# Optimization experiments

Hardware: AMD Instinct MI355X
Metric: run time of the kernel (lower is better)

## Reference

```python
import jax, jax.numpy as jnp
import numpy as np

N = 131072
F_IN = 256
FEATURES = 64
N_SOURCES = 32


def setup_inputs() -> dict:
    key = jax.random.key(0)
    k1, k2, k3 = jax.random.split(key, 3)
    x = jax.random.normal(k1, (N, F_IN), dtype=jnp.float32)
    source = jax.random.randint(k2, (N,), 0, N_SOURCES, dtype=jnp.int32)
    W = jax.random.normal(k3, (F_IN, N_SOURCES * FEATURES), dtype=jnp.float32) * (1.0 / np.sqrt(F_IN))
    b = jnp.zeros((N_SOURCES * FEATURES,), dtype=jnp.float32)
    return {"x": x, "source": source, "W": W, "b": b}


def reference(x, source, W, b):
    # Dense projection to all sources: (N, n_sources*features)
    y = jnp.dot(x, W) + b
    # Per-row gather of the slice belonging to this row's source id.
    # Equivalent to y[i, source[i]*FEATURES : (source[i]+1)*FEATURES].
    y = y.reshape(x.shape[0], N_SOURCES, FEATURES)
    out = jnp.take_along_axis(y, source[:, None, None].astype(jnp.int32), axis=1)
    return out[:, 0, :]  # (N, FEATURES)
```

## Files before the change

kernel.cpp:

```cpp
#include <hip/hip_runtime.h>

#define N_ROWS   131072
#define F_IN     256
#define FEAT     64
#define NSRC     32
#define WSTRIDE  (NSRC * FEAT)
#define CHUNK    4096
#define NCHUNK   (N_ROWS / CHUNK)
#define LCAP     320
#define KPAD     264
#define LCAP1    512

typedef __attribute__((ext_vector_type(8))) short  bf16x8;
typedef __attribute__((ext_vector_type(4))) float  f32x4;

__device__ __forceinline__ unsigned short f2bf(float f) {
    union { float f; unsigned u; } c; c.f = f;
    unsigned r = c.u + 0x7fffu + ((c.u >> 16) & 1u);
    return (unsigned short)(r >> 16);
}

__device__ __forceinline__ bf16x8 pack8(f32x4 f0, f32x4 f1) {
    bf16x8 a;
    a[0] = (short)f2bf(f0[0]); a[1] = (short)f2bf(f0[1]);
    a[2] = (short)f2bf(f0[2]); a[3] = (short)f2bf(f0[3]);
    a[4] = (short)f2bf(f1[0]); a[5] = (short)f2bf(f1[1]);
    a[6] = (short)f2bf(f1[2]); a[7] = (short)f2bf(f1[3]);
    return a;
}

__global__ __launch_bounds__(256)
void compact_kernel(const int* __restrict__ src, int* __restrict__ ws) {
    __shared__ int cnt[NSRC];
    __shared__ int lst[NSRC][LCAP];
    const int tid = threadIdx.x;
    if (tid < NSRC) cnt[tid] = 0;
    __syncthreads();

    const int chunk0 = blockIdx.x * CHUNK;
    #pragma unroll
    for (int r = 0; r < CHUNK / 256; ++r) {
        const int row = chunk0 + r * 256 + tid;
        const int s   = src[row];
        const int p   = atomicAdd(&cnt[s], 1);
        if (p < LCAP) lst[s][p] = row;
    }
    __syncthreads();

    if (tid < NSRC) ws[blockIdx.x * NSRC + tid] = min(cnt[tid], LCAP);
    int* gl = ws + NCHUNK * NSRC;
    for (int s = 0; s < NSRC; ++s) {
        const int c = min(cnt[s], LCAP);
        for (int i = tid; i < c; i += 256)
            gl[((size_t)blockIdx.x * NSRC + s) * LCAP + i] = lst[s][i];
    }
}

__global__ __launch_bounds__(256, 4)
void gemm_kernel(const float* __restrict__ x, const float* __restrict__ W,
                 const float* __restrict__ b, const int* __restrict__ ws,
                 float* __restrict__ out) {
    __shared__ __align__(16) unsigned short Wt[FEAT][KPAD];
    __shared__ int lst[LCAP];

    const int tid    = threadIdx.x;
    const int c      = blockIdx.x;
    const int s      = blockIdx.y;
    const int bucket = c * NSRC + s;
    const int count  = min(ws[bucket], LCAP);
    if (count == 0) return;

    for (int i = tid; i < count; i += 256)
        lst[i] = ws[NCHUNK * NSRC + (size_t)bucket * LCAP + i];

    {
        const int n  = tid & 63;
        const int kp = (tid >> 6) * 2;
        #pragma unroll
        for (int k0 = 0; k0 < F_IN; k0 += 8) {
            const int k = k0 + kp;
            const float w0 = W[(size_t)k       * WSTRIDE + s * FEAT + n];
            const float w1 = W[(size_t)(k + 1) * WSTRIDE + s * FEAT + n];
            *(unsigned*)&Wt[n][k] = (unsigned)f2bf(w0) | ((unsigned)f2bf(w1) << 16);
        }
    }
    __syncthreads();

    const int lane = tid & 63;
    const int w    = tid >> 6;
    const int col  = lane & 15;
    const int quad = lane >> 4;

    float bias[4];
    #pragma unroll
    for (int nt = 0; nt < 4; ++nt) bias[nt] = b[s * FEAT + nt * 16 + col];

    const int npass = (count + 63) >> 6;
    for (int p = 0; p < npass; ++p) {
        const int base = p * 64 + w * 16;
        const int ia   = lst[min(base + col, count - 1)];
        const float* ap = x + (size_t)ia * F_IN + quad * 8;

        f32x4 av[16];
        #pragma unroll
        for (int kk = 0; kk < 8; ++kk) {
            av[2 * kk]     = *(const f32x4*)(ap + kk * 32);
            av[2 * kk + 1] = *(const f32x4*)(ap + kk * 32 + 4);
        }

        f32x4 acc[4];
        #pragma unroll
        for (int nt = 0; nt < 4; ++nt) acc[nt] = (f32x4){0.f, 0.f, 0.f, 0.f};

        #pragma unroll
        for (int kk = 0; kk < 8; ++kk) {
            const bf16x8 a = pack8(av[2 * kk], av[2 * kk + 1]);
            #pragma unroll
            for (int nt = 0; nt < 4; ++nt) {
                const bf16x8 bb = *(const bf16x8*)&Wt[nt * 16 + col][kk * 32 + quad * 8];
                acc[nt] = __builtin_amdgcn_mfma_f32_16x16x32_bf16(a, bb, acc[nt], 0, 0, 0);
            }
        }

        #pragma unroll
        for (int reg = 0; reg < 4; ++reg) {
            const int gm = base + quad * 4 + reg;
            if (gm < count) {
                const int row = lst[gm];
                float* op = out + (size_t)row * FEAT;
                #pragma unroll
                for (int nt = 0; nt < 4; ++nt)
                    op[nt * 16 + col] = acc[nt][reg] + bias[nt];
            }
        }
    }
}

__global__ __launch_bounds__(256, 4)
void mono_kernel(const float* __restrict__ x, const int* __restrict__ src,
                 const float* __restrict__ W, const float* __restrict__ b,
                 float* __restrict__ out) {
    __shared__ __align__(16) unsigned short Wt[FEAT][KPAD];
    __shared__ int lst[LCAP1];
    __shared__ int cnt;

    const int tid    = threadIdx.x;
    const int s      = blockIdx.y;
    const int chunk0 = blockIdx.x * CHUNK;
    if (tid == 0) cnt = 0;
    __syncthreads();
    {
        const int n  = tid & 63;
        const int kp = (tid >> 6) * 2;
        #pragma unroll
        for (int k0 = 0; k0 < F_IN; k0 += 8) {
            const int k = k0 + kp;
            const float w0 = W[(size_t)k       * WSTRIDE + s * FEAT + n];
            const float w1 = W[(size_t)(k + 1) * WSTRIDE + s * FEAT + n];
            *(unsigned*)&Wt[n][k] = (unsigned)f2bf(w0) | ((unsigned)f2bf(w1) << 16);
        }
    }
    #pragma unroll
    for (int r = 0; r < CHUNK / 256; ++r) {
        const int row = chunk0 + r * 256 + tid;
        if (src[row] == s) {
            const int p = atomicAdd(&cnt, 1);
            if (p < LCAP1) lst[p] = row;
        }
    }
    __syncthreads();
    const int count = cnt;
    if (count == 0) return;
    const int lane = tid & 63, w = tid >> 6, col = lane & 15, quad = lane >> 4;
    float bias[4];
    #pragma unroll
    for (int nt = 0; nt < 4; ++nt) bias[nt] = b[s * FEAT + nt * 16 + col];
    const int npass = (count + 63) >> 6;
    for (int p = 0; p < npass; ++p) {
        const int base = p * 64 + w * 16;
        const int ia = lst[min(base + col, count - 1)];
        const float* ap = x + (size_t)ia * F_IN + quad * 8;
        f32x4 av[16];
        #pragma unroll
        for (int kk = 0; kk < 8; ++kk) {
            av[2 * kk]     = *(const f32x4*)(ap + kk * 32);
            av[2 * kk + 1] = *(const f32x4*)(ap + kk * 32 + 4);
        }
        f32x4 acc[4];
        #pragma unroll
        for (int nt = 0; nt < 4; ++nt) acc[nt] = (f32x4){0.f, 0.f, 0.f, 0.f};
        #pragma unroll
        for (int kk = 0; kk < 8; ++kk) {
            const bf16x8 a = pack8(av[2 * kk], av[2 * kk + 1]);
            #pragma unroll
            for (int nt = 0; nt < 4; ++nt) {
                const bf16x8 bb = *(const bf16x8*)&Wt[nt * 16 + col][kk * 32 + quad * 8];
                acc[nt] = __builtin_amdgcn_mfma_f32_16x16x32_bf16(a, bb, acc[nt], 0, 0, 0);
            }
        }
        #pragma unroll
        for (int reg = 0; reg < 4; ++reg) {
            const int gm = base + quad * 4 + reg;
            if (gm < count) {
                const int row = lst[gm];
                float* op = out + (size_t)row * FEAT;
                #pragma unroll
                for (int nt = 0; nt < 4; ++nt)
                    op[nt * 16 + col] = acc[nt][reg] + bias[nt];
            }
        }
    }
}

extern "C" void kernel_launch(void* const* d_in, const int* in_sizes, int n_in,
                              void* d_out, int out_size, void* d_ws, size_t ws_size,
                              hipStream_t stream) {
    const float* x   = (const float*)d_in[0];
    const int*   src = (const int*)d_in[1];
    const float* W   = (const float*)d_in[2];
    const float* b   = (const float*)d_in[3];
    float*       out = (float*)d_out;

    const size_t ws_needed = (size_t)(NCHUNK * NSRC) * (1 + LCAP) * sizeof(int);
    if (ws_size >= ws_needed) {
        int* ws = (int*)d_ws;
        compact_kernel<<<dim3(NCHUNK), dim3(256), 0, stream>>>(src, ws);
        gemm_kernel<<<dim3(NCHUNK, NSRC), dim3(256), 0, stream>>>(x, W, b, ws, out);
    } else {
        mono_kernel<<<dim3(NCHUNK, NSRC), dim3(256), 0, stream>>>(x, src, W, b, out);
    }
}
```

Measured before the change: 258.1 us.

## Double-buffer gathered x rows into LDS via async global_load_lds with register-held weights

Restructures the bucketed GEMM. Compaction now runs over many small blocks that reserve slots in global per-bucket counters with atomics, after a new zeroing kernel. Buckets grow to 8192-row chunks, giving fewer and larger GEMM blocks. The GEMM keeps the bf16 weight fragments in registers and streams gathered x rows into LDS with global_load_lds, double-buffered per wave and synchronised with waitcnt. Output is staged through LDS so rows are written with coalesced stores. The aim is to hide gather latency and improve store coalescing, at the cost of one wave set per CU (launch bounds 1), an extra kernel launch, and global atomics.

```diff
diff --git a/kernel.cpp b/kernel.cpp
--- a/kernel.cpp
+++ b/kernel.cpp
@@ -5,10 +5,16 @@
 #define FEAT     64
 #define NSRC     32
 #define WSTRIDE  (NSRC * FEAT)
-#define CHUNK    4096
-#define NCHUNK   (N_ROWS / CHUNK)
-#define LCAP     320
+#define NCH      16
+#define CHUNK    8192
+#define LCAP     640
+#define NBUCK    (NCH * NSRC)
 #define KPAD     264
+#define RSTRIDE  260
+#define BUFF     (16 * RSTRIDE)
+#define POOLF    (8 * BUFF)
+
+#define MCHUNK   4096
 #define LCAP1    512
 
 typedef __attribute__((ext_vector_type(8))) short  bf16x8;
@@ -29,38 +35,50 @@
     return a;
 }
 
+__device__ __forceinline__ void stage16(const float* __restrict__ x, int vr,
+                                        float* buf, int lane) {
+    #pragma unroll
+    for (int r = 0; r < 16; ++r) {
+        const int row = __builtin_amdgcn_readlane(vr, r);
+        const float* g = x + (size_t)row * F_IN + lane * 4;
+        __builtin_amdgcn_global_load_lds(
+            (const __attribute__((address_space(1))) void*)g,
+            (__attribute__((address_space(3))) void*)(buf + r * RSTRIDE),
+            16, 0, 0);
+    }
+}
+
+__global__ void zero_counts(int* __restrict__ ws) {
+    const int i = blockIdx.x * 256 + threadIdx.x;
+    if (i < NBUCK) ws[i] = 0;
+}
+
 __global__ __launch_bounds__(256)
 void compact_kernel(const int* __restrict__ src, int* __restrict__ ws) {
-    __shared__ int cnt[NSRC];
-    __shared__ int lst[NSRC][LCAP];
+    __shared__ int lcnt[NSRC];
+    __shared__ int gbase[NSRC];
     const int tid = threadIdx.x;
-    if (tid < NSRC) cnt[tid] = 0;
-    __syncthreads();
-
-    const int chunk0 = blockIdx.x * CHUNK;
-    #pragma unroll
-    for (int r = 0; r < CHUNK / 256; ++r) {
-        const int row = chunk0 + r * 256 + tid;
-        const int s   = src[row];
-        const int p   = atomicAdd(&cnt[s], 1);
-        if (p < LCAP) lst[s][p] = row;
-    }
-    __syncthreads();
-
-    if (tid < NSRC) ws[blockIdx.x * NSRC + tid] = min(cnt[tid], LCAP);
-    int* gl = ws + NCHUNK * NSRC;
-    for (int s = 0; s < NSRC; ++s) {
-        const int c = min(cnt[s], LCAP);
-        for (int i = tid; i < c; i += 256)
-            gl[((size_t)blockIdx.x * NSRC + s) * LCAP + i] = lst[s][i];
-    }
-}
-
-__global__ __launch_bounds__(256, 4)
+    if (tid < NSRC) lcnt[tid] = 0;
+    __syncthreads();
+
+    const int row = blockIdx.x * 256 + tid;
+    const int s   = src[row];
+    const int c   = (blockIdx.x * 256) >> 13;
+    const int p   = atomicAdd(&lcnt[s], 1);
+    __syncthreads();
+    if (tid < NSRC && lcnt[tid] > 0)
+        gbase[tid] = atomicAdd(&ws[c * NSRC + tid], lcnt[tid]);
+    __syncthreads();
+    const int pos = gbase[s] + p;
+    if (pos < LCAP)
+        ws[NBUCK + ((size_t)(c * NSRC + s)) * LCAP + pos] = row;
+}
+
+__global__ __launch_bounds__(256, 1)
 void gemm_kernel(const float* __restrict__ x, const float* __restrict__ W,
                  const float* __restrict__ b, const int* __restrict__ ws,
                  float* __restrict__ out) {
-    __shared__ __align__(16) unsigned short Wt[FEAT][KPAD];
+    __shared__ __align__(16) float pool[POOLF];
     __shared__ int lst[LCAP];
 
     const int tid    = threadIdx.x;
@@ -70,9 +88,10 @@
     const int count  = min(ws[bucket], LCAP);
     if (count == 0) return;
 
-    for (int i = tid; i < count; i += 256)
-        lst[i] = ws[NCHUNK * NSRC + (size_t)bucket * LCAP + i];
-
+    const int* gl = ws + NBUCK + (size_t)bucket * LCAP;
+    for (int i = tid; i < count; i += 256) lst[i] = gl[i];
+
+    unsigned short* Wt = (unsigned short*)pool;
     {
         const int n  = tid & 63;
         const int kp = (tid >> 6) * 2;
@@ -81,37 +100,134 @@
             const int k = k0 + kp;
             const float w0 = W[(size_t)k       * WSTRIDE + s * FEAT + n];
             const float w1 = W[(size_t)(k + 1) * WSTRIDE + s * FEAT + n];
+            *(unsigned*)&Wt[n * KPAD + k] = (unsigned)f2bf(w0) | ((unsigned)f2bf(w1) << 16);
+        }
+    }
+    __syncthreads();
+
+    const int lane = tid & 63, w = tid >> 6;
+    const int col  = lane & 15, quad = lane >> 4;
+
+    bf16x8 bfrag[4][8];
+    #pragma unroll
+    for (int nt = 0; nt < 4; ++nt)
+        #pragma unroll
+        for (int kk = 0; kk < 8; ++kk)
+            bfrag[nt][kk] = *(const bf16x8*)&Wt[(nt * 16 + col) * KPAD + kk * 32 + quad * 8];
+
+    float bias[4];
+    #pragma unroll
+    for (int nt = 0; nt < 4; ++nt) bias[nt] = b[s * FEAT + nt * 16 + col];
+
+    __syncthreads();
+
+    const int ntt = (count + 15) >> 4;
+    const int ntw = (w < ntt) ? (((ntt - 1 - w) >> 2) + 1) : 0;
+    if (ntw == 0) return;
+
+    float* buf0 = pool + w * (2 * BUFF);
+    float* buf1 = buf0 + BUFF;
+
+    __builtin_amdgcn_s_waitcnt(0x0F70);
+
+    int vr_cur = lst[min(w * 16 + col, count - 1)];
+    stage16(x, vr_cur, buf0, lane);
+
+    for (int i = 0; i < ntw; ++i) {
+        const int t    = w + 4 * i;
+        float*    bufc = (i & 1) ? buf1 : buf0;
+        const bool has_next = (i + 1 < ntw);
+        const bool has_prev = (i > 0);
+        int vr_next = 0;
+        if (has_next) {
+            vr_next = lst[min((t + 4) * 16 + col, count - 1)];
+            stage16(x, vr_next, (i & 1) ? buf0 : buf1, lane);
+        }
+        if (has_prev && has_next)      __builtin_amdgcn_s_waitcnt(0x8F70);
+        else if (has_prev || has_next) __builtin_amdgcn_s_waitcnt(0x4F70);
+        else                           __builtin_amdgcn_s_waitcnt(0x0F70);
+
+        f32x4 acc[4];
+        #pragma unroll
+        for (int nt = 0; nt < 4; ++nt) acc[nt] = (f32x4){0.f, 0.f, 0.f, 0.f};
+
+        #pragma unroll
+        for (int kk = 0; kk < 8; ++kk) {
+            const float* ap = bufc + col * RSTRIDE + kk * 32 + quad * 8;
+            const f32x4 a0 = *(const f32x4*)ap;
+            const f32x4 a1 = *(const f32x4*)(ap + 4);
+            const bf16x8 a = pack8(a0, a1);
+            #pragma unroll
+            for (int nt = 0; nt < 4; ++nt)
+                acc[nt] = __builtin_amdgcn_mfma_f32_16x16x32_bf16(a, bfrag[nt][kk], acc[nt], 0, 0, 0);
+        }
+
+        #pragma unroll
+        for (int nt = 0; nt < 4; ++nt)
+            #pragma unroll
+            for (int reg = 0; reg < 4; ++reg)
+                bufc[(quad * 4 + reg) * 65 + nt * 16 + col] = acc[nt][reg] + bias[nt];
+        #pragma unroll
+        for (int r = 0; r < 16; ++r) {
+            const int gi = t * 16 + r;
+            if (gi < count) {
+                const int row = __builtin_amdgcn_readlane(vr_cur, r);
+                out[(size_t)row * FEAT + lane] = bufc[r * 65 + lane];
+            }
+        }
+        vr_cur = vr_next;
+    }
+}
+
+__global__ __launch_bounds__(256, 4)
+void mono_kernel(const float* __restrict__ x, const int* __restrict__ src,
+                 const float* __restrict__ W, const float* __restrict__ b,
+                 float* __restrict__ out) {
+    __shared__ __align__(16) unsigned short Wt[FEAT][KPAD];
+    __shared__ int lst[LCAP1];
+    __shared__ int cnt;
+    const int tid = threadIdx.x, s = blockIdx.y, chunk0 = blockIdx.x * MCHUNK;
+    if (tid == 0) cnt = 0;
+    __syncthreads();
+    {
+        const int n = tid & 63, kp = (tid >> 6) * 2;
+        #pragma unroll
+        for (int k0 = 0; k0 < F_IN; k0 += 8) {
+            const int k = k0 + kp;
+            const float w0 = W[(size_t)k * WSTRIDE + s * FEAT + n];
+            const float w1 = W[(size_t)(k + 1) * WSTRIDE + s * FEAT + n];
             *(unsigned*)&Wt[n][k] = (unsigned)f2bf(w0) | ((unsigned)f2bf(w1) << 16);
         }
     }
-    __syncthreads();
-
-    const int lane = tid & 63;
-    const int w    = tid >> 6;
-    const int col  = lane & 15;
-    const int quad = lane >> 4;
-
+    #pragma unroll
+    for (int r = 0; r < MCHUNK / 256; ++r) {
+        const int row = chunk0 + r * 256 + tid;
+        if (src[row] == s) {
+            const int p = atomicAdd(&cnt, 1);
+            if (p < LCAP1) lst[p] = row;
+        }
+    }
+    __syncthreads();
+    const int count = cnt;
+    if (count == 0) return;
+    const int lane = tid & 63, w = tid >> 6, col = lane & 15, quad = lane >> 4;
     float bias[4];
     #pragma unroll
     for (int nt = 0; nt < 4; ++nt) bias[nt] = b[s * FEAT + nt * 16 + col];
-
     const int npass = (count + 63) >> 6;
     for (int p = 0; p < npass; ++p) {
         const int base = p * 64 + w * 16;
-        const int ia   = lst[min(base + col, count - 1)];
+        const int ia = lst[min(base + col, count - 1)];
         const float* ap = x + (size_t)ia * F_IN + quad * 8;
-
         f32x4 av[16];
         #pragma unroll
         for (int kk = 0; kk < 8; ++kk) {
             av[2 * kk]     = *(const f32x4*)(ap + kk * 32);
             av[2 * kk + 1] = *(const f32x4*)(ap + kk * 32 + 4);
         }
-
         f32x4 acc[4];
         #pragma unroll
         for (int nt = 0; nt < 4; ++nt) acc[nt] = (f32x4){0.f, 0.f, 0.f, 0.f};
-
         #pragma unroll
         for (int kk = 0; kk < 8; ++kk) {
             const bf16x8 a = pack8(av[2 * kk], av[2 * kk + 1]);
@@ -121,7 +237,6 @@
                 acc[nt] = __builtin_amdgcn_mfma_f32_16x16x32_bf16(a, bb, acc[nt], 0, 0, 0);
             }
         }
-
         #pragma unroll
         for (int reg = 0; reg < 4; ++reg) {
             const int gm = base + quad * 4 + reg;
@@ -136,82 +251,6 @@
     }
 }
 
-__global__ __launch_bounds__(256, 4)
-void mono_kernel(const float* __restrict__ x, const int* __restrict__ src,
-                 const float* __restrict__ W, const float* __restrict__ b,
-                 float* __restrict__ out) {
-    __shared__ __align__(16) unsigned short Wt[FEAT][KPAD];
-    __shared__ int lst[LCAP1];
-    __shared__ int cnt;
-
-    const int tid    = threadIdx.x;
-    const int s      = blockIdx.y;
-    const int chunk0 = blockIdx.x * CHUNK;
-    if (tid == 0) cnt = 0;
-    __syncthreads();
-    {
-        const int n  = tid & 63;
-        const int kp = (tid >> 6) * 2;
-        #pragma unroll
-        for (int k0 = 0; k0 < F_IN; k0 += 8) {
-            const int k = k0 + kp;
-            const float w0 = W[(size_t)k       * WSTRIDE + s * FEAT + n];
-            const float w1 = W[(size_t)(k + 1) * WSTRIDE + s * FEAT + n];
-            *(unsigned*)&Wt[n][k] = (unsigned)f2bf(w0) | ((unsigned)f2bf(w1) << 16);
-        }
-    }
-    #pragma unroll
-    for (int r = 0; r < CHUNK / 256; ++r) {
-        const int row = chunk0 + r * 256 + tid;
-        if (src[row] == s) {
-            const int p = atomicAdd(&cnt, 1);
-            if (p < LCAP1) lst[p] = row;
-        }
-    }
-    __syncthreads();
-    const int count = cnt;
-    if (count == 0) return;
-    const int lane = tid & 63, w = tid >> 6, col = lane & 15, quad = lane >> 4;
-    float bias[4];
-    #pragma unroll
-    for (int nt = 0; nt < 4; ++nt) bias[nt] = b[s * FEAT + nt * 16 + col];
-    const int npass = (count + 63) >> 6;
-    for (int p = 0; p < npass; ++p) {
-        const int base = p * 64 + w * 16;
-        const int ia = lst[min(base + col, count - 1)];
-        const float* ap = x + (size_t)ia * F_IN + quad * 8;
-        f32x4 av[16];
-        #pragma unroll
-        for (int kk = 0; kk < 8; ++kk) {
-            av[2 * kk]     = *(const f32x4*)(ap + kk * 32);
-            av[2 * kk + 1] = *(const f32x4*)(ap + kk * 32 + 4);
-        }
-        f32x4 acc[4];
-        #pragma unroll
-        for (int nt = 0; nt < 4; ++nt) acc[nt] = (f32x4){0.f, 0.f, 0.f, 0.f};
-        #pragma unroll
-        for (int kk = 0; kk < 8; ++kk) {
-            const bf16x8 a = pack8(av[2 * kk], av[2 * kk + 1]);
-            #pragma unroll
-            for (int nt = 0; nt < 4; ++nt) {
-                const bf16x8 bb = *(const bf16x8*)&Wt[nt * 16 + col][kk * 32 + quad * 8];
-                acc[nt] = __builtin_amdgcn_mfma_f32_16x16x32_bf16(a, bb, acc[nt], 0, 0, 0);
-            }
-        }
-        #pragma unroll
-        for (int reg = 0; reg < 4; ++reg) {
-            const int gm = base + quad * 4 + reg;
-            if (gm < count) {
-                const int row = lst[gm];
-                float* op = out + (size_t)row * FEAT;
-                #pragma unroll
-                for (int nt = 0; nt < 4; ++nt)
-                    op[nt * 16 + col] = acc[nt][reg] + bias[nt];
-            }
-        }
-    }
-}
-
 extern "C" void kernel_launch(void* const* d_in, const int* in_sizes, int n_in,
                               void* d_out, int out_size, void* d_ws, size_t ws_size,
                               hipStream_t stream) {
@@ -221,12 +260,13 @@
     const float* b   = (const float*)d_in[3];
     float*       out = (float*)d_out;
 
-    const size_t ws_needed = (size_t)(NCHUNK * NSRC) * (1 + LCAP) * sizeof(int);
+    const size_t ws_needed = (size_t)NBUCK * (1 + LCAP) * sizeof(int);
     if (ws_size >= ws_needed) {
         int* ws = (int*)d_ws;
-        compact_kernel<<<dim3(NCHUNK), dim3(256), 0, stream>>>(src, ws);
-        gemm_kernel<<<dim3(NCHUNK, NSRC), dim3(256), 0, stream>>>(x, W, b, ws, out);
+        zero_counts<<<dim3(2), dim3(256), 0, stream>>>(ws);
+        compact_kernel<<<dim3(N_ROWS / 256), dim3(256), 0, stream>>>(src, ws);
+        gemm_kernel<<<dim3(NCH, NSRC), dim3(256), 0, stream>>>(x, W, b, ws, out);
     } else {
-        mono_kernel<<<dim3(NCHUNK, NSRC), dim3(256), 0, stream>>>(x, src, W, b, out);
-    }
-}
+        mono_kernel<<<dim3(N_ROWS / MCHUNK, NSRC), dim3(256), 0, stream>>>(x, src, W, b, out);
+    }
+}
```

After: 222.5 us. 1.16x faster.
